# Performance work log

Measured on AMD Instinct MI355X. Metric: run time of the kernel, lower is better.

Reference implementation:

```python
import jax, jax.numpy as jnp
import numpy as np

NEG_INF = -9e15  # matches torch's -9000000000000000.0 fill
ALPHA = 0.2      # LeakyReLU negative slope


def setup_inputs() -> dict:
    key = jax.random.key(0)
    k1, k2, k3, k4 = jax.random.split(key, 4)
    B, F, N, T, C = 16, 128, 256, 64, 64
    h = jax.random.normal(k1, (B, F, N, T), dtype=jnp.float32)
    adj = jax.random.randint(k2, (B, N, N), 0, 2, dtype=jnp.int32)
    W = jax.random.normal(k3, (B, F, C), dtype=jnp.float32)
    a = jax.random.normal(k4, (B, 2 * C, 1), dtype=jnp.float32)
    return {"h": h, "adj": adj, "W": W, "a": a}


def reference(h, adj, W, a):
    # Wh: (B, C, N, T)
    Wh = jnp.einsum('bfnt,bfc->bcnt', h, W)
    C = W.shape[-1]
    # The original builds the O(N^2) pairwise concat then contracts with a.
    # Equivalently: e[b,i,j,t] = leakyrelu(a1.Wh[:, i] + a2.Wh[:, j])
    a1 = a[:, :C, 0]   # (B, C)
    a2 = a[:, C:, 0]   # (B, C)
    f = jnp.einsum('bcnt,bc->bnt', Wh, a1)  # (B, N, T)
    g = jnp.einsum('bcnt,bc->bnt', Wh, a2)  # (B, N, T)
    e = jax.nn.leaky_relu(f[:, :, None, :] + g[:, None, :, :], negative_slope=ALPHA)  # (B,N,N,T)
    mask = adj[:, :, :, None] > 0  # (B, N, N, 1) broadcast over T
    e = jnp.where(mask, e, NEG_INF)
    attention = jax.nn.softmax(e, axis=2)  # softmax over neighbor index m
    # dropout = 0.0 (eval-mode reference), so skipped
    h_prime = jnp.einsum('bnmt,bcmt->bcnt', attention, Wh)
    return jax.nn.elu(h_prime)  # concat=True branch
```

## Files before the change

### kernel.cpp

```cpp
#include <hip/hip_runtime.h>

#define B_ 16
#define F_ 128
#define N_ 256
#define T_ 64
#define C_ 64
#define ALPHA_ 0.2f
#define L2E_ 1.4426950408889634f

typedef short bf16x8 __attribute__((ext_vector_type(8)));
typedef float f32x4 __attribute__((ext_vector_type(4)));

__device__ __forceinline__ unsigned short f2bf(float x){
  unsigned int u = __float_as_uint(x);
  unsigned int r = u + 0x7FFFu + ((u >> 16) & 1u);
  return (unsigned short)(r >> 16);
}
__device__ __forceinline__ unsigned pk2(float a, float b){
  return ((unsigned)f2bf(b) << 16) | (unsigned)f2bf(a);
}
__device__ __forceinline__ unsigned sbit(unsigned w, int j){
  return (unsigned)(((int)(w << (31 - j))) >> 31);
}

__global__ void k_u(const float* __restrict__ W, const float* __restrict__ a,
                    float* __restrict__ u){
  int b = blockIdx.x, f = threadIdx.x;
  const float* Wb = W + (b*F_ + f)*C_;
  const float* ab = a + b*2*C_;
  float s1 = 0.f, s2 = 0.f;
#pragma unroll 8
  for (int c = 0; c < C_; ++c){
    float w = Wb[c];
    s1 = fmaf(w, ab[c], s1);
    s2 = fmaf(w, ab[C_ + c], s2);
  }
  u[b*F_ + f] = s1;
  u[B_*F_ + b*F_ + f] = s2;
}

__global__ void k_mask(const int* __restrict__ adj, unsigned* __restrict__ amask){
  int blk = blockIdx.x;
  int b = blk >> 2, r0 = (blk & 3)*64;
  int w = threadIdx.x >> 6, l = threadIdx.x & 63;
  const int* ab = adj + ((size_t)b*N_ + r0 + w*16)*N_;
  unsigned* om = amask + ((size_t)b*N_ + r0 + w*16)*8;
  for (int r = 0; r < 16; ++r){
    unsigned long long m0 = __ballot(ab[r*N_ +       l] > 0);
    unsigned long long m1 = __ballot(ab[r*N_ +  64 + l] > 0);
    unsigned long long m2 = __ballot(ab[r*N_ + 128 + l] > 0);
    unsigned long long m3 = __ballot(ab[r*N_ + 192 + l] > 0);
    if (l == 0){
      *(uint4*)(om + r*8)     = make_uint4((unsigned)m0, (unsigned)(m0>>32),
                                           (unsigned)m1, (unsigned)(m1>>32));
      *(uint4*)(om + r*8 + 4) = make_uint4((unsigned)m2, (unsigned)(m2>>32),
                                           (unsigned)m3, (unsigned)(m3>>32));
    }
  }
}

__global__ __launch_bounds__(256, 4) void k_wh(const float* __restrict__ h,
    const float* __restrict__ W, const float* __restrict__ u,
    unsigned short* __restrict__ wht, float* __restrict__ fvec,
    float* __restrict__ gvec){
  __shared__ uint4 hT4[1024];
  __shared__ uint4 wT4[1024];
  __shared__ float fpart[4][T_];
  __shared__ float gpart[4][T_];
  char* hT = (char*)hT4;
  char* wT = (char*)wT4;

  int bid = blockIdx.x, b = bid >> 8, n = bid & 255;
  int tid = threadIdx.x, w = tid >> 6, l = tid & 63;
  const float* hg = h + (size_t)b*F_*N_*T_ + n*T_;
  const float* Wg = W + b*F_*C_;
  const float* u1 = u + b*F_;
  const float* u2 = u + B_*F_ + b*F_;

  float sf = 0.f, sg = 0.f;
#pragma unroll
  for (int p = 0; p < 4; ++p){
    int f0 = p*32 + w*8;
    float v[8], wv[8];
#pragma unroll
    for (int j = 0; j < 8; ++j){
      v[j]  = hg[(size_t)(f0+j)*(N_*T_) + l];
      wv[j] = Wg[(f0+j)*C_ + l];
      sf = fmaf(v[j], u1[f0+j], sf);
      sg = fmaf(v[j], u2[f0+j], sg);
    }
    uint4 ph = make_uint4(pk2(v[0],v[1]),  pk2(v[2],v[3]),  pk2(v[4],v[5]),  pk2(v[6],v[7]));
    uint4 pw = make_uint4(pk2(wv[0],wv[1]),pk2(wv[2],wv[3]),pk2(wv[4],wv[5]),pk2(wv[6],wv[7]));
    *(uint4*)(hT + ((l*256 + f0*2) ^ ((l & 7) << 4))) = ph;
    *(uint4*)(wT + ((l*256 + f0*2) ^ ((l & 7) << 4))) = pw;
  }
  fpart[w][l] = sf;
  gpart[w][l] = sg;
  __syncthreads();

  if (tid < T_){
    float f_ = (fpart[0][tid] + fpart[1][tid]) + (fpart[2][tid] + fpart[3][tid]);
    float g_ = (gpart[0][tid] + gpart[1][tid]) + (gpart[2][tid] + gpart[3][tid]);
    fvec[(b*T_ + tid)*N_ + n] = f_ * L2E_;
    gvec[(b*T_ + tid)*N_ + n] = g_ * L2E_;
  }

  int li = l & 15, g_ = l >> 4;
  bf16x8 afr[4];
#pragma unroll
  for (int ch = 0; ch < 4; ++ch){
    int c = w*16 + li;
    afr[ch] = *(bf16x8*)(wT + ((c*256 + (ch*32 + g_*8)*2) ^ ((c & 7) << 4)));
  }
  f32x4 acc[4];
#pragma unroll
  for (int tt = 0; tt < 4; ++tt) acc[tt] = (f32x4){0.f,0.f,0.f,0.f};
#pragma unroll
  for (int tt = 0; tt < 4; ++tt){
#pragma unroll
    for (int ch = 0; ch < 4; ++ch){
      int t = tt*16 + li;
      bf16x8 bfr = *(bf16x8*)(hT + ((t*256 + (ch*32 + g_*8)*2) ^ ((t & 7) << 4)));
      acc[tt] = __builtin_amdgcn_mfma_f32_16x16x32_bf16(afr[ch], bfr, acc[tt], 0, 0, 0);
    }
  }
  unsigned short* wb = wht + ((size_t)b*T_*N_ + n)*C_;
#pragma unroll
  for (int tt = 0; tt < 4; ++tt){
    int t = tt*16 + li;
    int c0 = w*16 + g_*4;
    unsigned q0 = pk2(acc[tt][0], acc[tt][1]);
    unsigned q1 = pk2(acc[tt][2], acc[tt][3]);
    *(uint2*)(wb + (size_t)t*(N_*C_) + c0) = make_uint2(q0, q1);
  }
}

__global__ __launch_bounds__(256, 4) void k_attn(
    unsigned short* wht,
    const unsigned* __restrict__ amask,
    const float* __restrict__ fvec,
    const float* __restrict__ gvec){
  __shared__ uint4 whsT4[2048];
  __shared__ float gs[N_];
  __shared__ float invs[N_];
  char* dstT = (char*)whsT4;

  int bid = blockIdx.x;
  int b = bid >> 6, t = bid & 63;
  int tid = threadIdx.x, w = tid >> 6, l = tid & 63;
  int li = l & 15, g_ = l >> 4;

  const float* gp = gvec + (size_t)(b*T_ + t)*N_;
  const float* fp = fvec + (size_t)(b*T_ + t)*N_;
  if (tid < 64){
    float4 gg4 = *(const float4*)(gp + tid*4);
    *(float4*)&gs[tid*4] = gg4;
  }

  const char* src = (const char*)(wht + (size_t)(b*T_ + t)*(N_*C_));
#pragma unroll
  for (int i = 0; i < 4; ++i){
    int q2 = tid + i*256;
    int m = (q2 >> 3)*2, c0 = (q2 & 7)*8;
    uint4 ra = *(const uint4*)(src + m*128 + c0*2);
    uint4 rb = *(const uint4*)(src + (m+1)*128 + c0*2);
    unsigned va[4] = {ra.x, ra.y, ra.z, ra.w};
    unsigned vb[4] = {rb.x, rb.y, rb.z, rb.w};
#pragma unroll
    for (int k = 0; k < 4; ++k){
      int c = c0 + 2*k;
      unsigned lo = __builtin_amdgcn_perm(vb[k], va[k], 0x05040100u);
      unsigned hi = __builtin_amdgcn_perm(vb[k], va[k], 0x07060302u);
      *(unsigned*)(dstT + ((( c   *512) + m*2) ^ (((c  ) & 7) << 4))) = lo;
      *(unsigned*)(dstT + ((((c+1)*512) + m*2) ^ (((c+1) & 7) << 4))) = hi;
    }
  }
  __syncthreads();

  const unsigned* mbase = amask + ((size_t)b*N_ + w*64 + li)*8;

  float fl2[4];
#pragma unroll
  for (int mt = 0; mt < 4; ++mt) fl2[mt] = fp[w*64 + mt*16 + li];

  float mg2[4] = {-1e30f, -1e30f, -1e30f, -1e30f};
#pragma unroll 1
  for (int ch = 0; ch < 8; ++ch){
    const float* gq = &gs[ch*32 + g_*8];
    float4 ga = *(const float4*)gq;
    float4 gb = *(const float4*)(gq + 4);
    float gg[8] = {ga.x, ga.y, ga.z, ga.w, gb.x, gb.y, gb.z, gb.w};
#pragma unroll
    for (int mt = 0; mt < 4; ++mt){
      unsigned wds = mbase[mt*128 + ch] >> (g_*8);
#pragma unroll
      for (int j = 0; j < 8; ++j){
        float cand = __uint_as_float(__float_as_uint(gg[j]) & sbit(wds, j));
        mg2[mt] = fmaxf(mg2[mt], cand);
      }
    }
  }
  float fme[4], fme2[4];
#pragma unroll
  for (int mt = 0; mt < 4; ++mt){
    float v = mg2[mt];
    v = fmaxf(v, __shfl_xor(v, 16));
    v = fmaxf(v, __shfl_xor(v, 32));
    float em  = fl2[mt] + v;
    float me2 = fmaxf(em, ALPHA_*em);
    fme[mt]  = fl2[mt] - me2;
    fme2[mt] = fmaf(fl2[mt], ALPHA_, -me2);
  }

  f32x4 acc[4][4];
#pragma unroll
  for (int mt = 0; mt < 4; ++mt)
#pragma unroll
    for (int nt = 0; nt < 4; ++nt)
      acc[mt][nt] = (f32x4){0.f, 0.f, 0.f, 0.f};
  float sums[4] = {0.f, 0.f, 0.f, 0.f};

#pragma unroll 1
  for (int ch = 0; ch < 8; ++ch){
    bf16x8 bfr[4];
#pragma unroll
    for (int nt = 0; nt < 4; ++nt){
      int c = nt*16 + li;
      bfr[nt] = *(bf16x8*)(dstT + ((c*512 + (ch*32 + g_*8)*2) ^ ((c & 7) << 4)));
    }
    const float* gq = &gs[ch*32 + g_*8];
    float4 ga = *(const float4*)gq;
    float4 gb = *(const float4*)(gq + 4);
    float gg[8] = {ga.x, ga.y, ga.z, ga.w, gb.x, gb.y, gb.z, gb.w};
#pragma unroll
    for (int mt = 0; mt < 4; ++mt){
      unsigned wds = mbase[mt*128 + ch] >> (g_*8);
      float wv[8];
#pragma unroll
      for (int j = 0; j < 8; ++j){
        float d1 = gg[j] + fme[mt];
        float d2 = fmaf(gg[j], ALPHA_, fme2[mt]);
        float p  = exp2f(fmaxf(d1, d2));
        float v  = __uint_as_float(__float_as_uint(p) & sbit(wds, j));
        sums[mt] += v;
        wv[j] = v;
      }
      unsigned pk0, pk1, pk2_, pk3;
      asm("v_cvt_pk_bf16_f32 %0, %1, %2" : "=v"(pk0)  : "v"(wv[0]), "v"(wv[1]));
      asm("v_cvt_pk_bf16_f32 %0, %1, %2" : "=v"(pk1)  : "v"(wv[2]), "v"(wv[3]));
      asm("v_cvt_pk_bf16_f32 %0, %1, %2" : "=v"(pk2_) : "v"(wv[4]), "v"(wv[5]));
      asm("v_cvt_pk_bf16_f32 %0, %1, %2" : "=v"(pk3)  : "v"(wv[6]), "v"(wv[7]));
      union { unsigned u[4]; bf16x8 v; } afu;
      afu.u[0] = pk0; afu.u[1] = pk1; afu.u[2] = pk2_; afu.u[3] = pk3;
#pragma unroll
      for (int nt = 0; nt < 4; ++nt)
        acc[mt][nt] = __builtin_amdgcn_mfma_f32_16x16x32_bf16(afu.v, bfr[nt], acc[mt][nt], 0, 0, 0);
    }
  }

#pragma unroll
  for (int mt = 0; mt < 4; ++mt){
    float s = sums[mt];
    s += __shfl_xor(s, 16);
    s += __shfl_xor(s, 32);
    if (g_ == 0) invs[w*64 + mt*16 + li] = 1.0f / s;
  }

  unsigned short* ob = wht + (size_t)(b*T_ + t)*(N_*C_) + (size_t)w*64*C_;
#pragma unroll
  for (int mt = 0; mt < 4; ++mt){
#pragma unroll
    for (int reg = 0; reg < 4; ++reg){
      int row = mt*16 + g_*4 + reg;
      float inv = invs[w*64 + row];
#pragma unroll
      for (int nt = 0; nt < 4; ++nt){
        float v = acc[mt][nt][reg] * inv;
        v = v > 0.f ? v : (__expf(v) - 1.f);
        ob[row*C_ + nt*16 + li] = f2bf(v);
      }
    }
  }
}

__global__ __launch_bounds__(256) void k_tr(const unsigned short* __restrict__ whtO,
                                            float* __restrict__ out){
  __shared__ float tile[64][65];
  int bid = blockIdx.x;
  int b = bid >> 8, n = bid & 255;
  int tid = threadIdx.x;
  const unsigned short* src = whtO + ((size_t)b*T_*N_ + n)*C_;
#pragma unroll
  for (int i = 0; i < 2; ++i){
    int idx = tid + i*256;
    int t = idx >> 3, c0 = (idx & 7)*8;
    uint4 v = *(const uint4*)(src + (size_t)t*(N_*C_) + c0);
    unsigned arr[4] = {v.x, v.y, v.z, v.w};
#pragma unroll
    for (int k = 0; k < 4; ++k){
      tile[c0+2*k  ][t] = __uint_as_float(arr[k] << 16);
      tile[c0+2*k+1][t] = __uint_as_float(arr[k] & 0xFFFF0000u);
    }
  }
  __syncthreads();
  float* ob = out + (size_t)b*C_*N_*T_ + n*T_;
#pragma unroll
  for (int i = 0; i < 4; ++i){
    int idx = tid + i*256;
    int c = idx >> 4, t0 = (idx & 15)*4;
    float4 v = make_float4(tile[c][t0], tile[c][t0+1], tile[c][t0+2], tile[c][t0+3]);
    *(float4*)(ob + (size_t)c*(N_*T_) + t0) = v;
  }
}

extern "C" void kernel_launch(void* const* d_in, const int* in_sizes, int n_in,
                              void* d_out, int out_size, void* d_ws, size_t ws_size,
                              hipStream_t stream){
  (void)in_sizes; (void)n_in; (void)out_size; (void)ws_size;
  const float* h   = (const float*)d_in[0];
  const int*   adj = (const int*)d_in[1];
  const float* W   = (const float*)d_in[2];
  const float* a   = (const float*)d_in[3];
  float* u    = (float*)d_ws;
  float* fvec = u + 2*B_*F_;
  float* gvec = fvec + B_*N_*T_;
  unsigned short* wht = (unsigned short*)(gvec + B_*N_*T_);
  unsigned* amask = (unsigned*)(wht + (size_t)B_*T_*N_*C_);

  k_u   <<<dim3(B_),      dim3(F_),  0, stream>>>(W, a, u);
  k_mask<<<dim3(B_*4),    dim3(256), 0, stream>>>(adj, amask);
  k_wh  <<<dim3(B_*N_),   dim3(256), 0, stream>>>(h, W, u, wht, fvec, gvec);
  k_attn<<<dim3(B_*T_),   dim3(256), 0, stream>>>(wht, amask, fvec, gvec);
  k_tr  <<<dim3(B_*N_),   dim3(256), 0, stream>>>(wht, (float*)d_out);
}
```

Baseline: 126.6 us.

## Restructure attention kernel loads, mask packing, LDS swizzle and staged output stores

```diff
diff --git a/kernel.cpp b/kernel.cpp
--- a/kernel.cpp
+++ b/kernel.cpp
@@ -21,6 +21,9 @@
 }
 __device__ __forceinline__ unsigned sbit(unsigned w, int j){
   return (unsigned)(((int)(w << (31 - j))) >> 31);
+}
+__device__ __forceinline__ int swzT(int c){
+  return ((c & 7) ^ ((c >> 3) & 7)) << 4;
 }
 
 __global__ void k_u(const float* __restrict__ W, const float* __restrict__ a,
@@ -101,8 +104,8 @@
   if (tid < T_){
     float f_ = (fpart[0][tid] + fpart[1][tid]) + (fpart[2][tid] + fpart[3][tid]);
     float g_ = (gpart[0][tid] + gpart[1][tid]) + (gpart[2][tid] + gpart[3][tid]);
-    fvec[(b*T_ + tid)*N_ + n] = f_ * L2E_;
-    gvec[(b*T_ + tid)*N_ + n] = g_ * L2E_;
+    fvec[(b*N_ + n)*T_ + tid] = f_ * L2E_;
+    gvec[(b*N_ + n)*T_ + tid] = g_ * L2E_;
   }
 
   int li = l & 15, g_ = l >> 4;
@@ -150,11 +153,17 @@
   int tid = threadIdx.x, w = tid >> 6, l = tid & 63;
   int li = l & 15, g_ = l >> 4;
 
-  const float* gp = gvec + (size_t)(b*T_ + t)*N_;
-  const float* fp = fvec + (size_t)(b*T_ + t)*N_;
-  if (tid < 64){
-    float4 gg4 = *(const float4*)(gp + tid*4);
-    *(float4*)&gs[tid*4] = gg4;
+  gs[tid] = gvec[(b*N_ + tid)*T_ + t];
+
+  uint4 mlo[4], mhi[4];
+  float fl2[4];
+#pragma unroll
+  for (int mt = 0; mt < 4; ++mt){
+    int n = w*64 + mt*16 + li;
+    const uint4* mp = (const uint4*)(amask + ((size_t)b*N_ + n)*8);
+    mlo[mt] = mp[0];
+    mhi[mt] = mp[1];
+    fl2[mt] = fvec[(b*N_ + n)*T_ + t];
   }
 
   const char* src = (const char*)(wht + (size_t)(b*T_ + t)*(N_*C_));
@@ -171,19 +180,25 @@
       int c = c0 + 2*k;
       unsigned lo = __builtin_amdgcn_perm(vb[k], va[k], 0x05040100u);
       unsigned hi = __builtin_amdgcn_perm(vb[k], va[k], 0x07060302u);
-      *(unsigned*)(dstT + ((( c   *512) + m*2) ^ (((c  ) & 7) << 4))) = lo;
-      *(unsigned*)(dstT + ((((c+1)*512) + m*2) ^ (((c+1) & 7) << 4))) = hi;
-    }
-  }
-  __syncthreads();
-
-  const unsigned* mbase = amask + ((size_t)b*N_ + w*64 + li)*8;
-
-  float fl2[4];
-#pragma unroll
-  for (int mt = 0; mt < 4; ++mt) fl2[mt] = fp[w*64 + mt*16 + li];
-
-  float mg2[4] = {-1e30f, -1e30f, -1e30f, -1e30f};
+      *(unsigned*)(dstT + ((c*512 + m*2)     ^ swzT(c)))   = lo;
+      *(unsigned*)(dstT + (((c+1)*512 + m*2) ^ swzT(c+1))) = hi;
+    }
+  }
+
+  unsigned pk[4][2];
+  unsigned selA = 0x0C0C0000u | ((unsigned)(g_ + 4) << 8) | (unsigned)g_;
+#pragma unroll
+  for (int mt = 0; mt < 4; ++mt){
+    unsigned t0 = __builtin_amdgcn_perm(mlo[mt].y, mlo[mt].x, selA);
+    unsigned t1 = __builtin_amdgcn_perm(mlo[mt].w, mlo[mt].z, selA);
+    pk[mt][0] = __builtin_amdgcn_perm(t1, t0, 0x05040100u);
+    unsigned t2 = __builtin_amdgcn_perm(mhi[mt].y, mhi[mt].x, selA);
+    unsigned t3 = __builtin_amdgcn_perm(mhi[mt].w, mhi[mt].z, selA);
+    pk[mt][1] = __builtin_amdgcn_perm(t3, t2, 0x05040100u);
+  }
+  __syncthreads();
+
+  float mg[4] = {0.f, 0.f, 0.f, 0.f};
 #pragma unroll 1
   for (int ch = 0; ch < 8; ++ch){
     const float* gq = &gs[ch*32 + g_*8];
@@ -192,24 +207,24 @@
     float gg[8] = {ga.x, ga.y, ga.z, ga.w, gb.x, gb.y, gb.z, gb.w};
 #pragma unroll
     for (int mt = 0; mt < 4; ++mt){
-      unsigned wds = mbase[mt*128 + ch] >> (g_*8);
+      unsigned word = pk[mt][ch >> 2];
 #pragma unroll
       for (int j = 0; j < 8; ++j){
-        float cand = __uint_as_float(__float_as_uint(gg[j]) & sbit(wds, j));
-        mg2[mt] = fmaxf(mg2[mt], cand);
+        float cand = __uint_as_float(__float_as_uint(gg[j]) & sbit(word, (ch & 3)*8 + j));
+        mg[mt] = fmaxf(mg[mt], cand);
       }
     }
   }
   float fme[4], fme2[4];
 #pragma unroll
   for (int mt = 0; mt < 4; ++mt){
-    float v = mg2[mt];
+    float v = mg[mt];
     v = fmaxf(v, __shfl_xor(v, 16));
     v = fmaxf(v, __shfl_xor(v, 32));
-    float em  = fl2[mt] + v;
-    float me2 = fmaxf(em, ALPHA_*em);
-    fme[mt]  = fl2[mt] - me2;
-    fme2[mt] = fmaf(fl2[mt], ALPHA_, -me2);
+    float em = fl2[mt] + v;
+    float M  = fmaxf(em, ALPHA_*em);
+    fme[mt]  = fl2[mt] - M;
+    fme2[mt] = fmaf(fl2[mt], ALPHA_, -M);
   }
 
   f32x4 acc[4][4];
@@ -218,7 +233,7 @@
 #pragma unroll
     for (int nt = 0; nt < 4; ++nt)
       acc[mt][nt] = (f32x4){0.f, 0.f, 0.f, 0.f};
-  float sums[4] = {0.f, 0.f, 0.f, 0.f};
+  float s0[4] = {0.f,0.f,0.f,0.f}, s1[4] = {0.f,0.f,0.f,0.f};
 
 #pragma unroll 1
   for (int ch = 0; ch < 8; ++ch){
@@ -226,7 +241,7 @@
 #pragma unroll
     for (int nt = 0; nt < 4; ++nt){
       int c = nt*16 + li;
-      bfr[nt] = *(bf16x8*)(dstT + ((c*512 + (ch*32 + g_*8)*2) ^ ((c & 7) << 4)));
+      bfr[nt] = *(bf16x8*)(dstT + ((c*512 + (ch*32 + g_*8)*2) ^ swzT(c)));
     }
     const float* gq = &gs[ch*32 + g_*8];
     float4 ga = *(const float4*)gq;
@@ -234,24 +249,24 @@
     float gg[8] = {ga.x, ga.y, ga.z, ga.w, gb.x, gb.y, gb.z, gb.w};
 #pragma unroll
     for (int mt = 0; mt < 4; ++mt){
-      unsigned wds = mbase[mt*128 + ch] >> (g_*8);
+      unsigned word = pk[mt][ch >> 2];
       float wv[8];
 #pragma unroll
       for (int j = 0; j < 8; ++j){
         float d1 = gg[j] + fme[mt];
         float d2 = fmaf(gg[j], ALPHA_, fme2[mt]);
         float p  = exp2f(fmaxf(d1, d2));
-        float v  = __uint_as_float(__float_as_uint(p) & sbit(wds, j));
-        sums[mt] += v;
+        float v  = __uint_as_float(__float_as_uint(p) & sbit(word, (ch & 3)*8 + j));
+        if (j < 4) s0[mt] += v; else s1[mt] += v;
         wv[j] = v;
       }
-      unsigned pk0, pk1, pk2_, pk3;
-      asm("v_cvt_pk_bf16_f32 %0, %1, %2" : "=v"(pk0)  : "v"(wv[0]), "v"(wv[1]));
-      asm("v_cvt_pk_bf16_f32 %0, %1, %2" : "=v"(pk1)  : "v"(wv[2]), "v"(wv[3]));
-      asm("v_cvt_pk_bf16_f32 %0, %1, %2" : "=v"(pk2_) : "v"(wv[4]), "v"(wv[5]));
-      asm("v_cvt_pk_bf16_f32 %0, %1, %2" : "=v"(pk3)  : "v"(wv[6]), "v"(wv[7]));
+      unsigned q0, q1, q2_, q3;
+      asm("v_cvt_pk_bf16_f32 %0, %1, %2" : "=v"(q0)  : "v"(wv[0]), "v"(wv[1]));
+      asm("v_cvt_pk_bf16_f32 %0, %1, %2" : "=v"(q1)  : "v"(wv[2]), "v"(wv[3]));
+      asm("v_cvt_pk_bf16_f32 %0, %1, %2" : "=v"(q2_) : "v"(wv[4]), "v"(wv[5]));
+      asm("v_cvt_pk_bf16_f32 %0, %1, %2" : "=v"(q3)  : "v"(wv[6]), "v"(wv[7]));
       union { unsigned u[4]; bf16x8 v; } afu;
-      afu.u[0] = pk0; afu.u[1] = pk1; afu.u[2] = pk2_; afu.u[3] = pk3;
+      afu.u[0] = q0; afu.u[1] = q1; afu.u[2] = q2_; afu.u[3] = q3;
 #pragma unroll
       for (int nt = 0; nt < 4; ++nt)
         acc[mt][nt] = __builtin_amdgcn_mfma_f32_16x16x32_bf16(afu.v, bfr[nt], acc[mt][nt], 0, 0, 0);
@@ -260,26 +275,38 @@
 
 #pragma unroll
   for (int mt = 0; mt < 4; ++mt){
-    float s = sums[mt];
+    float s = s0[mt] + s1[mt];
     s += __shfl_xor(s, 16);
     s += __shfl_xor(s, 32);
     if (g_ == 0) invs[w*64 + mt*16 + li] = 1.0f / s;
   }
 
-  unsigned short* ob = wht + (size_t)(b*T_ + t)*(N_*C_) + (size_t)w*64*C_;
+  __syncthreads();
+  char* outb = dstT;
 #pragma unroll
   for (int mt = 0; mt < 4; ++mt){
 #pragma unroll
     for (int reg = 0; reg < 4; ++reg){
-      int row = mt*16 + g_*4 + reg;
-      float inv = invs[w*64 + row];
+      int nloc = w*64 + mt*16 + g_*4 + reg;
+      float inv = invs[nloc];
 #pragma unroll
       for (int nt = 0; nt < 4; ++nt){
         float v = acc[mt][nt][reg] * inv;
         v = v > 0.f ? v : (__expf(v) - 1.f);
-        ob[row*C_ + nt*16 + li] = f2bf(v);
+        int c = nt*16 + li;
+        int byteo = nloc*128 + (((c >> 3) ^ (nloc & 7)) << 4) + (c & 7)*2;
+        *(unsigned short*)(outb + byteo) = f2bf(v);
       }
     }
+  }
+  __syncthreads();
+  unsigned short* ob = wht + (size_t)(b*T_ + t)*(N_*C_);
+#pragma unroll
+  for (int k = 0; k < 8; ++k){
+    int idx = tid + k*256;
+    int nloc = idx >> 3, slot = idx & 7;
+    uint4 vq = *(const uint4*)(outb + nloc*128 + ((slot ^ (nloc & 7)) << 4));
+    *(uint4*)((char*)ob + (size_t)idx*16) = vq;
   }
 }
 
```

New measurement: 135.6 us. 1.07x slower.
